# Performance work log

Measured on AMD Instinct MI355X. Metric: run time of the kernel, lower is better.

## Reference

```python
import jax, jax.numpy as jnp
import numpy as np

EMBED = 1024
DSTATE = 16
DCONV = 4
DTRANK = 64  # ceil(EMBED/16)
B = 2
T = 2048


def setup_inputs() -> dict:
    key = jax.random.key(0)
    ks = jax.random.split(key, 8)
    def w(k, shape, s=0.02):
        return jax.random.normal(k, shape, dtype=jnp.float32) * s
    return dict(
        x=jax.random.normal(ks[0], (B, T, EMBED), dtype=jnp.float32),
        in_proj_w=w(ks[1], (2 * EMBED, EMBED)), in_proj_b=jnp.zeros((2 * EMBED,), jnp.float32),
        conv_w=w(ks[2], (EMBED, 1, DCONV)), conv_b=jnp.zeros((EMBED,), jnp.float32),
        x_proj_w=w(ks[3], (DTRANK + 2 * DSTATE, EMBED)), x_proj_b=jnp.zeros((DTRANK + 2 * DSTATE,), jnp.float32),
        dt_proj_w=w(ks[4], (EMBED, DTRANK)), dt_proj_b=jnp.zeros((EMBED,), jnp.float32),
        A_log=jnp.log(jnp.arange(1, DSTATE + 1, dtype=jnp.float32))[None, :],  # (1,N) as in torch module
        D_param=jnp.ones((EMBED,), jnp.float32),
        out_proj_w=w(ks[5], (EMBED, EMBED)), out_proj_b=jnp.zeros((EMBED,), jnp.float32),
        skip_proj_w=w(ks[6], (EMBED, EMBED)), skip_proj_b=jnp.zeros((EMBED,), jnp.float32),
    )


def reference(x, in_proj_w, in_proj_b, conv_w, conv_b, x_proj_w, x_proj_b,
              dt_proj_w, dt_proj_b, A_log, D_param, out_proj_w, out_proj_b,
              skip_proj_w, skip_proj_b):
    Bsz, Tlen, Dm = x.shape
    # in_proj and split into ssm branch and gate branch
    xr = x @ in_proj_w.T + in_proj_b            # (B,T,2D)
    x_in, res = jnp.split(xr, 2, axis=-1)
    # depthwise causal conv1d (torch pads both sides then slices [:T] == left-pad)
    xc = jax.lax.conv_general_dilated(
        x_in.transpose(0, 2, 1), conv_w, (1,), [(DCONV - 1, 0)],
        dimension_numbers=('NCH', 'OIH', 'NCH'), feature_group_count=Dm)
    xc = (xc + conv_b[None, :, None]).transpose(0, 2, 1)  # (B,T,D)
    xc = jax.nn.silu(xc)
    # input-dependent SSM params
    ssm = xc @ x_proj_w.T + x_proj_b            # (B,T,dt_rank+2N)
    delta, Bp, Cp = jnp.split(ssm, [DTRANK, DTRANK + DSTATE], axis=-1)
    delta = jax.nn.softplus(delta @ dt_proj_w.T + dt_proj_b)  # (B,T,D)
    A = -jnp.exp(A_log)                          # (1,N)
    dA = jnp.exp(delta[..., None] * A)           # (B,T,D,N)
    dBu = delta[..., None] * Bp[:, :, None, :] * xc[..., None]  # (B,T,D,N)
    # inclusive associative scan over time: h_t = dA_t * h_{t-1} + dBu_t
    def op(l, r):
        Ai, Bi = l
        Aj, Bj = r
        return (Aj * Ai, Bj + Aj * Bi)
    _, ys = jax.lax.associative_scan(op, (dA, dBu), axis=1)
    y = (ys * Cp[:, :, None, :]).sum(-1)         # (B,T,D)
    y = y + xc * D_param
    y = y * jax.nn.silu(res)
    return y @ out_proj_w.T + out_proj_b + (x @ skip_proj_w.T + skip_proj_b)
```

## Files before the change

kernel.cpp:

```cpp
#include <hip/hip_runtime.h>
#include <math.h>

#define EMBED  1024
#define DSTATE 16
#define DCONV  4
#define DTRANK 64
#define BB     2
#define TT     2048
#define M_TOK  (BB*TT)
#define SSMW   96
#define NCHUNK 64
#define CLEN   (TT/NCHUNK)

typedef __attribute__((ext_vector_type(8))) __bf16 bf16x8;
typedef __attribute__((ext_vector_type(4))) float floatx4;

__device__ __forceinline__ float silu_f(float x) {
    return x / (1.0f + __expf(-x));
}
__device__ __forceinline__ float softplus_f(float x) {
    return fmaxf(x, 0.0f) + log1pf(__expf(-fabsf(x)));
}
__device__ __forceinline__ unsigned short f2bf(float f) {
    union { float f; unsigned int u; } v; v.f = f;
    unsigned int u = v.u;
    return (unsigned short)((u + 0x7fffu + ((u >> 16) & 1u)) >> 16);
}
__device__ __forceinline__ float bf2f(unsigned short s) {
    union { unsigned int u; float f; } v; v.u = ((unsigned int)s) << 16;
    return v.f;
}
__device__ __forceinline__ void async16(unsigned short* lds, const unsigned short* g) {
    __builtin_amdgcn_global_load_lds(
        (const __attribute__((address_space(1))) unsigned int*)g,
        (__attribute__((address_space(3))) unsigned int*)lds, 16, 0, 0);
}

template<int EPI>
__global__ __launch_bounds__(256)
void gemm_bf16(const unsigned short* __restrict__ A, int lda,
               const unsigned short* __restrict__ W, int ldw,
               const float* __restrict__ bias, const float* __restrict__ bias2,
               float* __restrict__ C, int ldc, int K,
               unsigned short* __restrict__ aux)
{
    __shared__ unsigned short As[128 * 32];
    __shared__ unsigned short Ws[128 * 32];

    const int tid  = threadIdx.x;
    const int m0   = blockIdx.y * 128;
    const int n0   = blockIdx.x * 128;
    const int wid  = tid >> 6;
    const int lane = tid & 63;
    const int wm   = wid >> 1, wn = wid & 1;
    const int lr   = lane & 15;
    const int lq   = lane >> 4;

    const int l0 = tid,        row0 = l0 >> 2, kc0 = (l0 & 3) * 8;
    const int l1 = tid + 256,  row1 = l1 >> 2, kc1 = (l1 & 3) * 8;

    floatx4 acc[4][4] = {};

    for (int kt = 0; kt < K; kt += 32) {
        async16(&As[l0 * 8], A + (size_t)(m0 + row0) * lda + kt + kc0);
        async16(&As[l1 * 8], A + (size_t)(m0 + row1) * lda + kt + kc1);
        async16(&Ws[l0 * 8], W + (size_t)(n0 + row0) * ldw + kt + kc0);
        async16(&Ws[l1 * 8], W + (size_t)(n0 + row1) * ldw + kt + kc1);
        __syncthreads();

        bf16x8 af[4], bfr[4];
        #pragma unroll
        for (int i = 0; i < 4; ++i)
            af[i] = *(const bf16x8*)&As[(wm * 64 + i * 16 + lr) * 32 + lq * 8];
        #pragma unroll
        for (int i = 0; i < 4; ++i)
            bfr[i] = *(const bf16x8*)&Ws[(wn * 64 + i * 16 + lr) * 32 + lq * 8];

        #pragma unroll
        for (int mi = 0; mi < 4; ++mi)
            #pragma unroll
            for (int ni = 0; ni < 4; ++ni)
                acc[mi][ni] = __builtin_amdgcn_mfma_f32_16x16x32_bf16(
                    af[mi], bfr[ni], acc[mi][ni], 0, 0, 0);
        __syncthreads();
    }

    #pragma unroll
    for (int mi = 0; mi < 4; ++mi) {
        #pragma unroll
        for (int ni = 0; ni < 4; ++ni) {
            int nb = n0 + wn * 64 + ni * 16 + lr;
            #pragma unroll
            for (int r = 0; r < 4; ++r) {
                int m = m0 + wm * 64 + mi * 16 + lq * 4 + r;
                float v = acc[mi][ni][r];
                if (EPI == 0) {
                    C[(size_t)m * ldc + nb] = v + bias[nb];
                } else if (EPI == 1) {
                    if (nb < SSMW) {
                        float o = v + bias[nb];
                        C[(size_t)m * SSMW + nb] = o;
                        if (nb < DTRANK) aux[(size_t)m * DTRANK + nb] = f2bf(o);
                    }
                } else if (EPI == 2) {
                    aux[(size_t)m * ldc + nb] = f2bf(softplus_f(v + bias[nb]));
                } else {
                    C[(size_t)m * ldc + nb] = v + bias[nb] + bias2[nb];
                }
            }
        }
    }
}

__global__ __launch_bounds__(256)
void cvt_f32_bf16(const float* __restrict__ src, unsigned short* __restrict__ dst, int n)
{
    int i = (blockIdx.x * 256 + threadIdx.x) * 4;
    if (i >= n) return;
    float4 v = *(const float4*)&src[i];
    ushort4 o = { f2bf(v.x), f2bf(v.y), f2bf(v.z), f2bf(v.w) };
    *(ushort4*)&dst[i] = o;
}

__global__ __launch_bounds__(256)
void cvt_pad_xp(const float* __restrict__ src, unsigned short* __restrict__ dst)
{
    int i = (blockIdx.x * 256 + threadIdx.x) * 4;
    if (i >= 128 * EMBED) return;
    int row = i >> 10;
    ushort4 o = { 0, 0, 0, 0 };
    if (row < SSMW) {
        float4 v = *(const float4*)&src[i];
        o = { f2bf(v.x), f2bf(v.y), f2bf(v.z), f2bf(v.w) };
    }
    *(ushort4*)&dst[i] = o;
}

__global__ __launch_bounds__(256)
void cvt_cat_w(const float* __restrict__ ow, const float* __restrict__ sw,
               unsigned short* __restrict__ dst)
{
    int i = (blockIdx.x * 256 + threadIdx.x) * 4;
    if (i >= EMBED * 2 * EMBED) return;
    int n = i >> 11, k = i & 2047;
    const float* s = (k < EMBED) ? &ow[(size_t)n * EMBED + k]
                                 : &sw[(size_t)n * EMBED + (k - EMBED)];
    float4 v = *(const float4*)s;
    ushort4 o = { f2bf(v.x), f2bf(v.y), f2bf(v.z), f2bf(v.w) };
    *(ushort4*)&dst[i] = o;
}

__global__ __launch_bounds__(256)
void cvt_x(const float* __restrict__ x, unsigned short* __restrict__ Acat)
{
    int i = (blockIdx.x * 256 + threadIdx.x) * 4;
    if (i >= M_TOK * EMBED) return;
    int m = i >> 10, k = i & 1023;
    float4 v = *(const float4*)&x[i];
    ushort4 o = { f2bf(v.x), f2bf(v.y), f2bf(v.z), f2bf(v.w) };
    *(ushort4*)&Acat[(size_t)m * 2 * EMBED + EMBED + k] = o;
}

__global__ __launch_bounds__(256)
void conv_silu_kernel(const float* __restrict__ xr,
                      const float* __restrict__ conv_w,
                      const float* __restrict__ conv_b,
                      unsigned short* __restrict__ xcb)
{
    int idx = blockIdx.x * blockDim.x + threadIdx.x;
    if (idx >= BB * TT * EMBED) return;
    int d = idx & (EMBED - 1);
    int t = (idx >> 10) & (TT - 1);
    int b = idx >> 21;

    float w0 = conv_w[d * 4 + 0];
    float w1 = conv_w[d * 4 + 1];
    float w2 = conv_w[d * 4 + 2];
    float w3 = conv_w[d * 4 + 3];

    size_t base = ((size_t)(b * TT + t)) * (2 * EMBED) + d;
    float s = conv_b[d];
    if (t >= 3) s = fmaf(w0, xr[base - 3 * 2 * EMBED], s);
    if (t >= 2) s = fmaf(w1, xr[base - 2 * 2 * EMBED], s);
    if (t >= 1) s = fmaf(w2, xr[base - 1 * 2 * EMBED], s);
    s = fmaf(w3, xr[base], s);
    xcb[(size_t)(b * TT + t) * EMBED + d] = f2bf(silu_f(s));
}

__global__ __launch_bounds__(256)
void scan_chunk_kernel(const unsigned short* __restrict__ deltab,
                       const unsigned short* __restrict__ xcb,
                       const float* __restrict__ ssm,
                       const float* __restrict__ A_log,
                       float* __restrict__ hio,
                       float* __restrict__ Ssum)
{
    __shared__ float Bs[CLEN][DSTATE];
    const int tid = threadIdx.x;
    const int blk = blockIdx.x;
    const int dg = blk & 3, chunk = (blk >> 2) & (NCHUNK - 1), b = blk >> 8;
    const int d = dg * 256 + tid;
    const int t0 = chunk * CLEN;

    for (int i = tid; i < CLEN * DSTATE; i += 256) {
        int t = i >> 4, n = i & 15;
        Bs[t][n] = ssm[(size_t)(b * TT + t0 + t) * SSMW + DTRANK + n];
    }
    __syncthreads();

    float An[DSTATE];
    #pragma unroll
    for (int n = 0; n < DSTATE; ++n) An[n] = -__expf(A_log[n]);

    float h[DSTATE] = {};
    float S = 0.f;
    for (int t = 0; t < CLEN; ++t) {
        size_t row = (size_t)(b * TT + t0 + t);
        float dv = bf2f(deltab[row * EMBED + d]);
        float xv = bf2f(xcb[row * EMBED + d]);
        S += dv;
        float sx = dv * xv;
        float Bv[DSTATE];
        *(float4*)&Bv[0]  = *(const float4*)&Bs[t][0];
        *(float4*)&Bv[4]  = *(const float4*)&Bs[t][4];
        *(float4*)&Bv[8]  = *(const float4*)&Bs[t][8];
        *(float4*)&Bv[12] = *(const float4*)&Bs[t][12];
        #pragma unroll
        for (int n = 0; n < DSTATE; ++n) {
            float dA = __expf(dv * An[n]);
            h[n] = fmaf(dA, h[n], sx * Bv[n]);
        }
    }
    size_t base = ((size_t)(chunk * BB + b) * EMBED + d) * DSTATE;
    #pragma unroll
    for (int j = 0; j < 4; ++j)
        *(float4*)&hio[base + j * 4] = *(float4*)&h[j * 4];
    Ssum[(size_t)(chunk * BB + b) * EMBED + d] = S;
}

__global__ __launch_bounds__(256)
void scan_combine_kernel(const float* __restrict__ A_log,
                         const float* __restrict__ Ssum,
                         float* __restrict__ hio)
{
    int idx = blockIdx.x * 256 + threadIdx.x;
    int n  = idx & 15;
    int bd = idx >> 4;
    float An = -__expf(A_log[n]);
    float h = 0.f;
    for (int c = 0; c < NCHUNK; ++c) {
        size_t off = (size_t)c * (BB * EMBED * DSTATE) + idx;
        float ho = hio[off];
        float ap = __expf(An * Ssum[(size_t)c * (BB * EMBED) + bd]);
        hio[off] = h;
        h = fmaf(ap, h, ho);
    }
}

__global__ __launch_bounds__(256)
void scan_apply_kernel(const unsigned short* __restrict__ deltab,
                       const unsigned short* __restrict__ xcb,
                       const float* __restrict__ ssm,
                       const float* __restrict__ A_log,
                       const float* __restrict__ D_param,
                       const float* __restrict__ xr,
                       const float* __restrict__ hin,
                       unsigned short* __restrict__ Acat)
{
    __shared__ float Bs[CLEN][DSTATE];
    __shared__ float Cs[CLEN][DSTATE];
    const int tid = threadIdx.x;
    const int blk = blockIdx.x;
    const int dg = blk & 3, chunk = (blk >> 2) & (NCHUNK - 1), b = blk >> 8;
    const int d = dg * 256 + tid;
    const int t0 = chunk * CLEN;

    for (int i = tid; i < CLEN * DSTATE; i += 256) {
        int t = i >> 4, n = i & 15;
        size_t row = (size_t)(b * TT + t0 + t);
        Bs[t][n] = ssm[row * SSMW + DTRANK + n];
        Cs[t][n] = ssm[row * SSMW + DTRANK + DSTATE + n];
    }
    __syncthreads();

    float An[DSTATE];
    #pragma unroll
    for (int n = 0; n < DSTATE; ++n) An[n] = -__expf(A_log[n]);
    float Dd = D_param[d];

    float h[DSTATE];
    size_t base = ((size_t)(chunk * BB + b) * EMBED + d) * DSTATE;
    #pragma unroll
    for (int j = 0; j < 4; ++j)
        *(float4*)&h[j * 4] = *(const float4*)&hin[base + j * 4];

    for (int t = 0; t < CLEN; ++t) {
        size_t row = (size_t)(b * TT + t0 + t);
        float dv = bf2f(deltab[row * EMBED + d]);
        float xv = bf2f(xcb[row * EMBED + d]);
        float sx = dv * xv;
        float Bv[DSTATE], Cv[DSTATE];
        *(float4*)&Bv[0]  = *(const float4*)&Bs[t][0];
        *(float4*)&Bv[4]  = *(const float4*)&Bs[t][4];
        *(float4*)&Bv[8]  = *(const float4*)&Bs[t][8];
        *(float4*)&Bv[12] = *(const float4*)&Bs[t][12];
        *(float4*)&Cv[0]  = *(const float4*)&Cs[t][0];
        *(float4*)&Cv[4]  = *(const float4*)&Cs[t][4];
        *(float4*)&Cv[8]  = *(const float4*)&Cs[t][8];
        *(float4*)&Cv[12] = *(const float4*)&Cs[t][12];
        float y0 = 0.f, y1 = 0.f, y2 = 0.f, y3 = 0.f;
        #pragma unroll
        for (int n = 0; n < DSTATE; n += 4) {
            float dA0 = __expf(dv * An[n + 0]);
            float dA1 = __expf(dv * An[n + 1]);
            float dA2 = __expf(dv * An[n + 2]);
            float dA3 = __expf(dv * An[n + 3]);
            h[n + 0] = fmaf(dA0, h[n + 0], sx * Bv[n + 0]);
            h[n + 1] = fmaf(dA1, h[n + 1], sx * Bv[n + 1]);
            h[n + 2] = fmaf(dA2, h[n + 2], sx * Bv[n + 2]);
            h[n + 3] = fmaf(dA3, h[n + 3], sx * Bv[n + 3]);
            y0 = fmaf(h[n + 0], Cv[n + 0], y0);
            y1 = fmaf(h[n + 1], Cv[n + 1], y1);
            y2 = fmaf(h[n + 2], Cv[n + 2], y2);
            y3 = fmaf(h[n + 3], Cv[n + 3], y3);
        }
        float yv = (y0 + y1) + (y2 + y3) + xv * Dd;
        float rv = xr[row * (2 * EMBED) + EMBED + d];
        Acat[row * 2 * EMBED + d] = f2bf(yv * silu_f(rv));
    }
}

extern "C" void kernel_launch(void* const* d_in, const int* in_sizes, int n_in,
                              void* d_out, int out_size, void* d_ws, size_t ws_size,
                              hipStream_t stream) {
    const float* x      = (const float*)d_in[0];
    const float* in_w   = (const float*)d_in[1];
    const float* in_b   = (const float*)d_in[2];
    const float* conv_w = (const float*)d_in[3];
    const float* conv_b = (const float*)d_in[4];
    const float* xp_w   = (const float*)d_in[5];
    const float* xp_b   = (const float*)d_in[6];
    const float* dt_w   = (const float*)d_in[7];
    const float* dt_b   = (const float*)d_in[8];
    const float* A_log  = (const float*)d_in[9];
    const float* Dp     = (const float*)d_in[10];
    const float* out_w  = (const float*)d_in[11];
    const float* out_b  = (const float*)d_in[12];
    const float* skip_w = (const float*)d_in[13];
    const float* skip_b = (const float*)d_in[14];
    float* out = (float*)d_out;

    float* ws    = (float*)d_ws;
    float* xr    = ws;
    float* ssm   = xr   + (size_t)M_TOK * 2 * EMBED;
    float* hio   = ssm  + (size_t)M_TOK * SSMW;
    float* Ssum  = hio  + (size_t)NCHUNK * BB * EMBED * DSTATE;
    unsigned short* Acat = (unsigned short*)(Ssum + (size_t)NCHUNK * BB * EMBED);
    unsigned short* xcb  = Acat + (size_t)M_TOK * 2 * EMBED;
    unsigned short* dltb = xcb  + (size_t)M_TOK * EMBED;
    unsigned short* dtin = dltb + (size_t)M_TOK * EMBED;
    unsigned short* inwb = dtin + (size_t)M_TOK * DTRANK;
    unsigned short* xpwb = inwb + (size_t)2 * EMBED * EMBED;
    unsigned short* dtwb = xpwb + (size_t)128 * EMBED;
    unsigned short* wcat = dtwb + (size_t)EMBED * DTRANK;

    dim3 blk(256);

    cvt_f32_bf16<<<(2 * EMBED * EMBED / 4 + 255) / 256, blk, 0, stream>>>(in_w, inwb, 2 * EMBED * EMBED);
    cvt_f32_bf16<<<(EMBED * DTRANK / 4 + 255) / 256, blk, 0, stream>>>(dt_w, dtwb, EMBED * DTRANK);
    cvt_pad_xp<<<(128 * EMBED / 4 + 255) / 256, blk, 0, stream>>>(xp_w, xpwb);
    cvt_cat_w<<<(EMBED * 2 * EMBED / 4 + 255) / 256, blk, 0, stream>>>(out_w, skip_w, wcat);
    cvt_x<<<(M_TOK * EMBED / 4 + 255) / 256, blk, 0, stream>>>(x, Acat);

    gemm_bf16<0><<<dim3(2 * EMBED / 128, M_TOK / 128), blk, 0, stream>>>(
        Acat + EMBED, 2 * EMBED, inwb, EMBED, in_b, nullptr, xr, 2 * EMBED, EMBED, nullptr);

    conv_silu_kernel<<<(M_TOK * EMBED + 255) / 256, blk, 0, stream>>>(xr, conv_w, conv_b, xcb);

    gemm_bf16<1><<<dim3(1, M_TOK / 128), blk, 0, stream>>>(
        xcb, EMBED, xpwb, EMBED, xp_b, nullptr, ssm, SSMW, EMBED, dtin);

    gemm_bf16<2><<<dim3(EMBED / 128, M_TOK / 128), blk, 0, stream>>>(
        dtin, DTRANK, dtwb, DTRANK, dt_b, nullptr, nullptr, EMBED, DTRANK, dltb);

    scan_chunk_kernel<<<BB * NCHUNK * (EMBED / 256), blk, 0, stream>>>(
        dltb, xcb, ssm, A_log, hio, Ssum);
    scan_combine_kernel<<<(BB * EMBED * DSTATE + 255) / 256, blk, 0, stream>>>(
        A_log, Ssum, hio);
    scan_apply_kernel<<<BB * NCHUNK * (EMBED / 256), blk, 0, stream>>>(
        dltb, xcb, ssm, A_log, Dp, xr, hio, Acat);

    gemm_bf16<3><<<dim3(EMBED / 128, M_TOK / 128), blk, 0, stream>>>(
        Acat, 2 * EMBED, wcat, 2 * EMBED, out_b, skip_b, out, EMBED, 2 * EMBED, nullptr);
}
```

Baseline: 306.9 us.

## Split-K x_proj GEMM, fuse gate SiLU into in_proj, merge conversion kernels

The five weight and input conversion kernels become a single packed launch. The in_proj epilogue now writes the x branch as fp32 and the gate as bf16 SiLU values, so scan_apply reads a 2-byte gate and does no SiLU. The x_proj GEMM, which had only 32 blocks, is split along K into 8 slices with a merge kernel, giving more parallelism at the cost of extra partial-sum traffic. The conv kernel is vectorised to float4, scan_combine batches its loads and uses separate in/out buffers, and the GEMM grids swap to M-major block order.

```diff
diff --git a/kernel.cpp b/kernel.cpp
--- a/kernel.cpp
+++ b/kernel.cpp
@@ -11,6 +11,7 @@
 #define SSMW   96
 #define NCHUNK 64
 #define CLEN   (TT/NCHUNK)
+#define KSPLIT 8
 
 typedef __attribute__((ext_vector_type(8))) __bf16 bf16x8;
 typedef __attribute__((ext_vector_type(4))) float floatx4;
@@ -36,32 +37,24 @@
         (__attribute__((address_space(3))) unsigned int*)lds, 16, 0, 0);
 }
 
-template<int EPI>
-__global__ __launch_bounds__(256)
-void gemm_bf16(const unsigned short* __restrict__ A, int lda,
-               const unsigned short* __restrict__ W, int ldw,
-               const float* __restrict__ bias, const float* __restrict__ bias2,
-               float* __restrict__ C, int ldc, int K,
-               unsigned short* __restrict__ aux)
+#define GEMM_DECODE \
+    const int tid = threadIdx.x; const int wid = tid >> 6; \
+    const int lane = tid & 63; \
+    const int wm = wid >> 1, wn = wid & 1; \
+    const int lr = lane & 15; const int lq = lane >> 4;
+
+__device__ __forceinline__ void gemm_acc(
+    const unsigned short* __restrict__ A, int lda,
+    const unsigned short* __restrict__ W, int ldw,
+    int m0, int n0, int k0, int klen, floatx4 (&acc)[4][4])
 {
     __shared__ unsigned short As[128 * 32];
     __shared__ unsigned short Ws[128 * 32];
-
-    const int tid  = threadIdx.x;
-    const int m0   = blockIdx.y * 128;
-    const int n0   = blockIdx.x * 128;
-    const int wid  = tid >> 6;
-    const int lane = tid & 63;
-    const int wm   = wid >> 1, wn = wid & 1;
-    const int lr   = lane & 15;
-    const int lq   = lane >> 4;
-
-    const int l0 = tid,        row0 = l0 >> 2, kc0 = (l0 & 3) * 8;
-    const int l1 = tid + 256,  row1 = l1 >> 2, kc1 = (l1 & 3) * 8;
-
-    floatx4 acc[4][4] = {};
-
-    for (int kt = 0; kt < K; kt += 32) {
+    GEMM_DECODE;
+    const int l0 = tid,       row0 = l0 >> 2, kc0 = (l0 & 3) * 8;
+    const int l1 = tid + 256, row1 = l1 >> 2, kc1 = (l1 & 3) * 8;
+
+    for (int kt = k0; kt < k0 + klen; kt += 32) {
         async16(&As[l0 * 8], A + (size_t)(m0 + row0) * lda + kt + kc0);
         async16(&As[l1 * 8], A + (size_t)(m0 + row1) * lda + kt + kc1);
         async16(&Ws[l0 * 8], W + (size_t)(n0 + row0) * ldw + kt + kc0);
@@ -84,116 +77,212 @@
                     af[mi], bfr[ni], acc[mi][ni], 0, 0, 0);
         __syncthreads();
     }
-
-    #pragma unroll
-    for (int mi = 0; mi < 4; ++mi) {
+}
+
+__global__ __launch_bounds__(256)
+void gemm_in(const unsigned short* __restrict__ A,
+             const unsigned short* __restrict__ W,
+             const float* __restrict__ bias,
+             float* __restrict__ xr, unsigned short* __restrict__ gate)
+{
+    floatx4 acc[4][4] = {};
+    const int m0 = blockIdx.x * 128, n0 = blockIdx.y * 128;
+    gemm_acc(A, 2 * EMBED, W, EMBED, m0, n0, 0, EMBED, acc);
+    GEMM_DECODE;
+    #pragma unroll
+    for (int mi = 0; mi < 4; ++mi)
         #pragma unroll
         for (int ni = 0; ni < 4; ++ni) {
             int nb = n0 + wn * 64 + ni * 16 + lr;
             #pragma unroll
             for (int r = 0; r < 4; ++r) {
                 int m = m0 + wm * 64 + mi * 16 + lq * 4 + r;
-                float v = acc[mi][ni][r];
-                if (EPI == 0) {
-                    C[(size_t)m * ldc + nb] = v + bias[nb];
-                } else if (EPI == 1) {
-                    if (nb < SSMW) {
-                        float o = v + bias[nb];
-                        C[(size_t)m * SSMW + nb] = o;
-                        if (nb < DTRANK) aux[(size_t)m * DTRANK + nb] = f2bf(o);
-                    }
-                } else if (EPI == 2) {
-                    aux[(size_t)m * ldc + nb] = f2bf(softplus_f(v + bias[nb]));
-                } else {
-                    C[(size_t)m * ldc + nb] = v + bias[nb] + bias2[nb];
+                float v = acc[mi][ni][r] + bias[nb];
+                if (nb < EMBED) xr[(size_t)m * EMBED + nb] = v;
+                else gate[(size_t)m * EMBED + nb - EMBED] = f2bf(silu_f(v));
+            }
+        }
+}
+
+__global__ __launch_bounds__(256)
+void gemm_xp(const unsigned short* __restrict__ A,
+             const unsigned short* __restrict__ W,
+             float* __restrict__ xpart)
+{
+    floatx4 acc[4][4] = {};
+    const int m0 = blockIdx.x * 128;
+    const int k0 = blockIdx.z * (EMBED / KSPLIT);
+    gemm_acc(A, EMBED, W, EMBED, m0, 0, k0, EMBED / KSPLIT, acc);
+    GEMM_DECODE;
+    float* base = xpart + (size_t)blockIdx.z * M_TOK * SSMW;
+    #pragma unroll
+    for (int mi = 0; mi < 4; ++mi)
+        #pragma unroll
+        for (int ni = 0; ni < 4; ++ni) {
+            int nb = wn * 64 + ni * 16 + lr;
+            if (nb < SSMW) {
+                #pragma unroll
+                for (int r = 0; r < 4; ++r) {
+                    int m = m0 + wm * 64 + mi * 16 + lq * 4 + r;
+                    base[(size_t)m * SSMW + nb] = acc[mi][ni][r];
                 }
             }
         }
-    }
-}
-
-__global__ __launch_bounds__(256)
-void cvt_f32_bf16(const float* __restrict__ src, unsigned short* __restrict__ dst, int n)
-{
-    int i = (blockIdx.x * 256 + threadIdx.x) * 4;
-    if (i >= n) return;
-    float4 v = *(const float4*)&src[i];
+}
+
+__global__ __launch_bounds__(256)
+void xp_merge(const float* __restrict__ xpart, const float* __restrict__ xp_b,
+              float* __restrict__ ssm, unsigned short* __restrict__ dtin)
+{
+    int idx = blockIdx.x * 256 + threadIdx.x;
+    if (idx >= M_TOK * SSMW) return;
+    int m = idx / SSMW, n = idx - m * SSMW;
+    float s = xp_b[n];
+    #pragma unroll
+    for (int z = 0; z < KSPLIT; ++z) s += xpart[(size_t)z * M_TOK * SSMW + idx];
+    ssm[idx] = s;
+    if (n < DTRANK) dtin[(size_t)m * DTRANK + n] = f2bf(s);
+}
+
+__global__ __launch_bounds__(256)
+void gemm_dt(const unsigned short* __restrict__ A,
+             const unsigned short* __restrict__ W,
+             const float* __restrict__ bias,
+             unsigned short* __restrict__ dltb)
+{
+    floatx4 acc[4][4] = {};
+    const int m0 = blockIdx.x * 128, n0 = blockIdx.y * 128;
+    gemm_acc(A, DTRANK, W, DTRANK, m0, n0, 0, DTRANK, acc);
+    GEMM_DECODE;
+    #pragma unroll
+    for (int mi = 0; mi < 4; ++mi)
+        #pragma unroll
+        for (int ni = 0; ni < 4; ++ni) {
+            int nb = n0 + wn * 64 + ni * 16 + lr;
+            #pragma unroll
+            for (int r = 0; r < 4; ++r) {
+                int m = m0 + wm * 64 + mi * 16 + lq * 4 + r;
+                dltb[(size_t)m * EMBED + nb] = f2bf(softplus_f(acc[mi][ni][r] + bias[nb]));
+            }
+        }
+}
+
+__global__ __launch_bounds__(256)
+void gemm_out(const unsigned short* __restrict__ A,
+              const unsigned short* __restrict__ W,
+              const float* __restrict__ bias, const float* __restrict__ bias2,
+              float* __restrict__ C)
+{
+    floatx4 acc[4][4] = {};
+    const int m0 = blockIdx.x * 128, n0 = blockIdx.y * 128;
+    gemm_acc(A, 2 * EMBED, W, 2 * EMBED, m0, n0, 0, 2 * EMBED, acc);
+    GEMM_DECODE;
+    #pragma unroll
+    for (int mi = 0; mi < 4; ++mi)
+        #pragma unroll
+        for (int ni = 0; ni < 4; ++ni) {
+            int nb = n0 + wn * 64 + ni * 16 + lr;
+            float bb = bias[nb] + bias2[nb];
+            #pragma unroll
+            for (int r = 0; r < 4; ++r) {
+                int m = m0 + wm * 64 + mi * 16 + lq * 4 + r;
+                C[(size_t)m * EMBED + nb] = acc[mi][ni][r] + bb;
+            }
+        }
+}
+
+#define SEG0 524288
+#define SEG1 (SEG0 + 16384)
+#define SEG2 (SEG1 + 32768)
+#define SEG3 (SEG2 + 524288)
+#define SEG4 (SEG3 + 1048576)
+
+__global__ __launch_bounds__(256)
+void cvt_pack(const float* __restrict__ in_w, const float* __restrict__ dt_w,
+              const float* __restrict__ xp_w, const float* __restrict__ ow,
+              const float* __restrict__ sw, const float* __restrict__ x,
+              unsigned short* __restrict__ inwb, unsigned short* __restrict__ dtwb,
+              unsigned short* __restrict__ xpwb, unsigned short* __restrict__ wcat,
+              unsigned short* __restrict__ Acat)
+{
+    int j = blockIdx.x * 256 + threadIdx.x;
+    if (j >= SEG4) return;
+    float4 v = {0.f, 0.f, 0.f, 0.f};
+    unsigned short* dst;
+    if (j < SEG0) {
+        v = *(const float4*)&in_w[j * 4];
+        dst = &inwb[j * 4];
+    } else if (j < SEG1) {
+        int i = (j - SEG0) * 4;
+        v = *(const float4*)&dt_w[i];
+        dst = &dtwb[i];
+    } else if (j < SEG2) {
+        int i = (j - SEG1) * 4;
+        if ((i >> 10) < SSMW) v = *(const float4*)&xp_w[i];
+        dst = &xpwb[i];
+    } else if (j < SEG3) {
+        int i = (j - SEG2) * 4;
+        int n = i >> 11, k = i & 2047;
+        v = *(const float4*)((k < EMBED) ? &ow[(size_t)n * EMBED + k]
+                                         : &sw[(size_t)n * EMBED + (k - EMBED)]);
+        dst = &wcat[i];
+    } else {
+        int i = (j - SEG3) * 4;
+        int m = i >> 10, k = i & 1023;
+        v = *(const float4*)&x[i];
+        dst = &Acat[(size_t)m * 2 * EMBED + EMBED + k];
+    }
     ushort4 o = { f2bf(v.x), f2bf(v.y), f2bf(v.z), f2bf(v.w) };
-    *(ushort4*)&dst[i] = o;
-}
-
-__global__ __launch_bounds__(256)
-void cvt_pad_xp(const float* __restrict__ src, unsigned short* __restrict__ dst)
-{
-    int i = (blockIdx.x * 256 + threadIdx.x) * 4;
-    if (i >= 128 * EMBED) return;
-    int row = i >> 10;
-    ushort4 o = { 0, 0, 0, 0 };
-    if (row < SSMW) {
-        float4 v = *(const float4*)&src[i];
-        o = { f2bf(v.x), f2bf(v.y), f2bf(v.z), f2bf(v.w) };
-    }
-    *(ushort4*)&dst[i] = o;
-}
-
-__global__ __launch_bounds__(256)
-void cvt_cat_w(const float* __restrict__ ow, const float* __restrict__ sw,
-               unsigned short* __restrict__ dst)
-{
-    int i = (blockIdx.x * 256 + threadIdx.x) * 4;
-    if (i >= EMBED * 2 * EMBED) return;
-    int n = i >> 11, k = i & 2047;
-    const float* s = (k < EMBED) ? &ow[(size_t)n * EMBED + k]
-                                 : &sw[(size_t)n * EMBED + (k - EMBED)];
-    float4 v = *(const float4*)s;
-    ushort4 o = { f2bf(v.x), f2bf(v.y), f2bf(v.z), f2bf(v.w) };
-    *(ushort4*)&dst[i] = o;
-}
-
-__global__ __launch_bounds__(256)
-void cvt_x(const float* __restrict__ x, unsigned short* __restrict__ Acat)
-{
-    int i = (blockIdx.x * 256 + threadIdx.x) * 4;
-    if (i >= M_TOK * EMBED) return;
-    int m = i >> 10, k = i & 1023;
-    float4 v = *(const float4*)&x[i];
-    ushort4 o = { f2bf(v.x), f2bf(v.y), f2bf(v.z), f2bf(v.w) };
-    *(ushort4*)&Acat[(size_t)m * 2 * EMBED + EMBED + k] = o;
-}
-
-__global__ __launch_bounds__(256)
-void conv_silu_kernel(const float* __restrict__ xr,
-                      const float* __restrict__ conv_w,
-                      const float* __restrict__ conv_b,
-                      unsigned short* __restrict__ xcb)
-{
-    int idx = blockIdx.x * blockDim.x + threadIdx.x;
-    if (idx >= BB * TT * EMBED) return;
-    int d = idx & (EMBED - 1);
-    int t = (idx >> 10) & (TT - 1);
-    int b = idx >> 21;
-
-    float w0 = conv_w[d * 4 + 0];
-    float w1 = conv_w[d * 4 + 1];
-    float w2 = conv_w[d * 4 + 2];
-    float w3 = conv_w[d * 4 + 3];
-
-    size_t base = ((size_t)(b * TT + t)) * (2 * EMBED) + d;
-    float s = conv_b[d];
-    if (t >= 3) s = fmaf(w0, xr[base - 3 * 2 * EMBED], s);
-    if (t >= 2) s = fmaf(w1, xr[base - 2 * 2 * EMBED], s);
-    if (t >= 1) s = fmaf(w2, xr[base - 1 * 2 * EMBED], s);
-    s = fmaf(w3, xr[base], s);
-    xcb[(size_t)(b * TT + t) * EMBED + d] = f2bf(silu_f(s));
-}
-
-__global__ __launch_bounds__(256)
-void scan_chunk_kernel(const unsigned short* __restrict__ deltab,
-                       const unsigned short* __restrict__ xcb,
-                       const float* __restrict__ ssm,
-                       const float* __restrict__ A_log,
-                       float* __restrict__ hio,
-                       float* __restrict__ Ssum)
+    *(ushort4*)dst = o;
+}
+
+__global__ __launch_bounds__(256)
+void conv_silu(const float* __restrict__ xr,
+               const float* __restrict__ conv_w,
+               const float* __restrict__ conv_b,
+               unsigned short* __restrict__ xcb)
+{
+    int idx = blockIdx.x * 256 + threadIdx.x;
+    if (idx >= BB * TT * EMBED / 4) return;
+    int dq = idx & (EMBED / 4 - 1);
+    int t  = (idx >> 8) & (TT - 1);
+    int b  = idx >> 19;
+    int d  = dq * 4;
+
+    float4 cw0 = *(const float4*)&conv_w[(d + 0) * 4];
+    float4 cw1 = *(const float4*)&conv_w[(d + 1) * 4];
+    float4 cw2 = *(const float4*)&conv_w[(d + 2) * 4];
+    float4 cw3 = *(const float4*)&conv_w[(d + 3) * 4];
+    float4 s   = *(const float4*)&conv_b[d];
+
+    const float* w0 = (const float*)&cw0;
+    const float* w1 = (const float*)&cw1;
+    const float* w2 = (const float*)&cw2;
+    const float* w3 = (const float*)&cw3;
+
+    #pragma unroll
+    for (int jj = 0; jj < 4; ++jj) {
+        int tr = t - 3 + jj;
+        if (tr >= 0) {
+            float4 v = *(const float4*)&xr[(size_t)(b * TT + tr) * EMBED + d];
+            s.x = fmaf(w0[jj], v.x, s.x);
+            s.y = fmaf(w1[jj], v.y, s.y);
+            s.z = fmaf(w2[jj], v.z, s.z);
+            s.w = fmaf(w3[jj], v.w, s.w);
+        }
+    }
+    ushort4 o = { f2bf(silu_f(s.x)), f2bf(silu_f(s.y)),
+                  f2bf(silu_f(s.z)), f2bf(silu_f(s.w)) };
+    *(ushort4*)&xcb[(size_t)(b * TT + t) * EMBED + d] = o;
+}
+
+__global__ __launch_bounds__(256)
+void scan_chunk(const unsigned short* __restrict__ deltab,
+                const unsigned short* __restrict__ xcb,
+                const float* __restrict__ ssm,
+                const float* __restrict__ A_log,
+                float* __restrict__ hout,
+                float* __restrict__ Ssum)
 {
     __shared__ float Bs[CLEN][DSTATE];
     const int tid = threadIdx.x;
@@ -233,39 +322,46 @@
     }
     size_t base = ((size_t)(chunk * BB + b) * EMBED + d) * DSTATE;
     #pragma unroll
-    for (int j = 0; j < 4; ++j)
-        *(float4*)&hio[base + j * 4] = *(float4*)&h[j * 4];
+    for (int jj = 0; jj < 4; ++jj)
+        *(float4*)&hout[base + jj * 4] = *(float4*)&h[jj * 4];
     Ssum[(size_t)(chunk * BB + b) * EMBED + d] = S;
 }
 
 __global__ __launch_bounds__(256)
-void scan_combine_kernel(const float* __restrict__ A_log,
-                         const float* __restrict__ Ssum,
-                         float* __restrict__ hio)
+void scan_combine(const float* __restrict__ A_log,
+                  const float* __restrict__ Ssum,
+                  const float* __restrict__ hout,
+                  float* __restrict__ hin)
 {
     int idx = blockIdx.x * 256 + threadIdx.x;
     int n  = idx & 15;
     int bd = idx >> 4;
     float An = -__expf(A_log[n]);
     float h = 0.f;
-    for (int c = 0; c < NCHUNK; ++c) {
-        size_t off = (size_t)c * (BB * EMBED * DSTATE) + idx;
-        float ho = hio[off];
-        float ap = __expf(An * Ssum[(size_t)c * (BB * EMBED) + bd]);
-        hio[off] = h;
-        h = fmaf(ap, h, ho);
-    }
-}
-
-__global__ __launch_bounds__(256)
-void scan_apply_kernel(const unsigned short* __restrict__ deltab,
-                       const unsigned short* __restrict__ xcb,
-                       const float* __restrict__ ssm,
-                       const float* __restrict__ A_log,
-                       const float* __restrict__ D_param,
-                       const float* __restrict__ xr,
-                       const float* __restrict__ hin,
-                       unsigned short* __restrict__ Acat)
+    for (int c0 = 0; c0 < NCHUNK; c0 += 8) {
+        float ho[8], S[8];
+        #pragma unroll
+        for (int jj = 0; jj < 8; ++jj) {
+            ho[jj] = hout[(size_t)(c0 + jj) * (BB * EMBED * DSTATE) + idx];
+            S[jj]  = Ssum[(size_t)(c0 + jj) * (BB * EMBED) + bd];
+        }
+        #pragma unroll
+        for (int jj = 0; jj < 8; ++jj) {
+            hin[(size_t)(c0 + jj) * (BB * EMBED * DSTATE) + idx] = h;
+            h = fmaf(__expf(An * S[jj]), h, ho[jj]);
+        }
+    }
+}
+
+__global__ __launch_bounds__(256)
+void scan_apply(const unsigned short* __restrict__ deltab,
+                const unsigned short* __restrict__ xcb,
+                const float* __restrict__ ssm,
+                const float* __restrict__ A_log,
+                const float* __restrict__ D_param,
+                const unsigned short* __restrict__ gate,
+                const float* __restrict__ hin,
+                unsigned short* __restrict__ Acat)
 {
     __shared__ float Bs[CLEN][DSTATE];
     __shared__ float Cs[CLEN][DSTATE];
@@ -291,8 +387,8 @@
     float h[DSTATE];
     size_t base = ((size_t)(chunk * BB + b) * EMBED + d) * DSTATE;
     #pragma unroll
-    for (int j = 0; j < 4; ++j)
-        *(float4*)&h[j * 4] = *(const float4*)&hin[base + j * 4];
+    for (int jj = 0; jj < 4; ++jj)
+        *(float4*)&h[jj * 4] = *(const float4*)&hin[base + jj * 4];
 
     for (int t = 0; t < CLEN; ++t) {
         size_t row = (size_t)(b * TT + t0 + t);
@@ -325,8 +421,8 @@
             y3 = fmaf(h[n + 3], Cv[n + 3], y3);
         }
         float yv = (y0 + y1) + (y2 + y3) + xv * Dd;
-        float rv = xr[row * (2 * EMBED) + EMBED + d];
-        Acat[row * 2 * EMBED + d] = f2bf(yv * silu_f(rv));
+        float g = bf2f(gate[row * EMBED + d]);
+        Acat[row * 2 * EMBED + d] = f2bf(yv * g);
     }
 }
 
@@ -352,44 +448,45 @@
 
     float* ws    = (float*)d_ws;
     float* xr    = ws;
-    float* ssm   = xr   + (size_t)M_TOK * 2 * EMBED;
-    float* hio   = ssm  + (size_t)M_TOK * SSMW;
-    float* Ssum  = hio  + (size_t)NCHUNK * BB * EMBED * DSTATE;
+    float* ssm   = xr    + (size_t)M_TOK * EMBED;
+    float* xpart = ssm   + (size_t)M_TOK * SSMW;
+    float* hout  = xpart + (size_t)KSPLIT * M_TOK * SSMW;
+    float* hin   = hout  + (size_t)NCHUNK * BB * EMBED * DSTATE;
+    float* Ssum  = hin   + (size_t)NCHUNK * BB * EMBED * DSTATE;
     unsigned short* Acat = (unsigned short*)(Ssum + (size_t)NCHUNK * BB * EMBED);
     unsigned short* xcb  = Acat + (size_t)M_TOK * 2 * EMBED;
     unsigned short* dltb = xcb  + (size_t)M_TOK * EMBED;
     unsigned short* dtin = dltb + (size_t)M_TOK * EMBED;
-    unsigned short* inwb = dtin + (size_t)M_TOK * DTRANK;
+    unsigned short* gate = dtin + (size_t)M_TOK * DTRANK;
+    unsigned short* inwb = gate + (size_t)M_TOK * EMBED;
     unsigned short* xpwb = inwb + (size_t)2 * EMBED * EMBED;
     unsigned short* dtwb = xpwb + (size_t)128 * EMBED;
     unsigned short* wcat = dtwb + (size_t)EMBED * DTRANK;
 
     dim3 blk(256);
 
-    cvt_f32_bf16<<<(2 * EMBED * EMBED / 4 + 255) / 256, blk, 0, stream>>>(in_w, inwb, 2 * EMBED * EMBED);
-    cvt_f32_bf16<<<(EMBED * DTRANK / 4 + 255) / 256, blk, 0, stream>>>(dt_w, dtwb, EMBED * DTRANK);
-    cvt_pad_xp<<<(128 * EMBED / 4 + 255) / 256, blk, 0, stream>>>(xp_w, xpwb);
-    cvt_cat_w<<<(EMBED * 2 * EMBED / 4 + 255) / 256, blk, 0, stream>>>(out_w, skip_w, wcat);
-    cvt_x<<<(M_TOK * EMBED / 4 + 255) / 256, blk, 0, stream>>>(x, Acat);
-
-    gemm_bf16<0><<<dim3(2 * EMBED / 128, M_TOK / 128), blk, 0, stream>>>(
-        Acat + EMBED, 2 * EMBED, inwb, EMBED, in_b, nullptr, xr, 2 * EMBED, EMBED, nullptr);
-
-    conv_silu_kernel<<<(M_TOK * EMBED + 255) / 256, blk, 0, stream>>>(xr, conv_w, conv_b, xcb);
-
-    gemm_bf16<1><<<dim3(1, M_TOK / 128), blk, 0, stream>>>(
-        xcb, EMBED, xpwb, EMBED, xp_b, nullptr, ssm, SSMW, EMBED, dtin);
-
-    gemm_bf16<2><<<dim3(EMBED / 128, M_TOK / 128), blk, 0, stream>>>(
-        dtin, DTRANK, dtwb, DTRANK, dt_b, nullptr, nullptr, EMBED, DTRANK, dltb);
-
-    scan_chunk_kernel<<<BB * NCHUNK * (EMBED / 256), blk, 0, stream>>>(
-        dltb, xcb, ssm, A_log, hio, Ssum);
-    scan_combine_kernel<<<(BB * EMBED * DSTATE + 255) / 256, blk, 0, stream>>>(
-        A_log, Ssum, hio);
-    scan_apply_kernel<<<BB * NCHUNK * (EMBED / 256), blk, 0, stream>>>(
-        dltb, xcb, ssm, A_log, Dp, xr, hio, Acat);
-
-    gemm_bf16<3><<<dim3(EMBED / 128, M_TOK / 128), blk, 0, stream>>>(
-        Acat, 2 * EMBED, wcat, 2 * EMBED, out_b, skip_b, out, EMBED, 2 * EMBED, nullptr);
-}
+    cvt_pack<<<(SEG4 + 255) / 256, blk, 0, stream>>>(
+        in_w, dt_w, xp_w, out_w, skip_w, x, inwb, dtwb, xpwb, wcat, Acat);
+
+    gemm_in<<<dim3(M_TOK / 128, 2 * EMBED / 128), blk, 0, stream>>>(
+        Acat + EMBED, inwb, in_b, xr, gate);
+
+    conv_silu<<<(M_TOK * EMBED / 4 + 255) / 256, blk, 0, stream>>>(
+        xr, conv_w, conv_b, xcb);
+
+    gemm_xp<<<dim3(M_TOK / 128, 1, KSPLIT), blk, 0, stream>>>(xcb, xpwb, xpart);
+    xp_merge<<<(M_TOK * SSMW + 255) / 256, blk, 0, stream>>>(xpart, xp_b, ssm, dtin);
+
+    gemm_dt<<<dim3(M_TOK / 128, EMBED / 128), blk, 0, stream>>>(
+        dtin, dtwb, dt_b, dltb);
+
+    scan_chunk<<<BB * NCHUNK * (EMBED / 256), blk, 0, stream>>>(
+        dltb, xcb, ssm, A_log, hout, Ssum);
+    scan_combine<<<(BB * EMBED * DSTATE + 255) / 256, blk, 0, stream>>>(
+        A_log, Ssum, hout, hin);
+    scan_apply<<<BB * NCHUNK * (EMBED / 256), blk, 0, stream>>>(
+        dltb, xcb, ssm, A_log, Dp, gate, hin, Acat);
+
+    gemm_out<<<dim3(M_TOK / 128, EMBED / 128), blk, 0, stream>>>(
+        Acat, wcat, out_b, skip_b, out);
+}
```

Result: faster. 278.9 us (-9.1%).
